# Kernel optimization log

Hardware: AMD Instinct MI355X
Metric: run time of the kernel (lower is better)

## Reference

```python
import jax, jax.numpy as jnp
import numpy as np

NEG_BIG = 1e9  # additive mask magnitude from the original code


def setup_inputs() -> dict:
    key = jax.random.key(0)
    k1, k2, k3 = jax.random.split(key, 3)
    B, H, W, Cqk, Cv = 4, 64, 64, 256, 256
    return {
        "query": jax.random.normal(k1, (B, H, W, Cqk), dtype=jnp.float32),
        "key": jax.random.normal(k2, (B, H, W, Cqk), dtype=jnp.float32),
        "value": jax.random.normal(k3, (B, H, W, Cv), dtype=jnp.float32),
    }


def reference(query, key, value):
    B = query.shape[0]
    Cqk = key.shape[-1]
    Cv = value.shape[-1]
    out_spatial = query.shape[1:-1]

    q = query.reshape(B, -1, Cqk)   # [B, Sq, C]
    k = key.reshape(B, -1, Cqk)     # [B, S, C]
    v = value.reshape(B, -1, Cv)    # [B, S, Cv]
    Sq = q.shape[1]

    # PixelSNAIL causal mask: position i may attend to strictly earlier
    # positions j < i (row 0 attends to nothing -> zero output row).
    allowed = jnp.tril(jnp.ones((Sq, Sq), dtype=q.dtype), k=-1)  # [Sq, S]

    scale = 1.0 / jnp.sqrt(jnp.asarray(Cqk, dtype=q.dtype))
    scores = jnp.einsum("bqc,bkc->bqk", q, k) * scale  # [B, Sq, S]
    scores = scores - NEG_BIG * (1.0 - allowed)
    probs = jax.nn.softmax(scores, axis=-1) * allowed   # zero out masked probs
    mixed = jnp.einsum("bqk,bkv->bqv", probs, v)        # [B, Sq, Cv]
    return mixed.reshape((B,) + out_spatial + (Cv,))
```

## Files before the change

### kernel.cpp

```cpp
#include <hip/hip_runtime.h>

#define S_LEN 4096
#define DIM   256
#define QBLK  128
#define KVBLK 64
#define TILE_SH (KVBLK * DIM)
#define PER_B  1056
#define NBLK   256

typedef __attribute__((ext_vector_type(4))) float f32x4;
typedef __attribute__((ext_vector_type(8))) short bf16x8;
typedef __attribute__((ext_vector_type(4))) unsigned short u16x4;
typedef __attribute__((ext_vector_type(8))) unsigned short u16x8;

__device__ __forceinline__ unsigned short f2bf(float x) {
    union { float f; unsigned u; } v; v.f = x;
    unsigned r = v.u + 0x7FFFu + ((v.u >> 16) & 1u);
    return (unsigned short)(r >> 16);
}
__device__ __forceinline__ float bf2f(unsigned short h) {
    union { unsigned u; float f; } v; v.u = ((unsigned)h) << 16;
    return v.f;
}

__device__ __forceinline__ void g2l16(const unsigned short* g, unsigned short* s) {
    __builtin_amdgcn_global_load_lds(
        (const __attribute__((address_space(1))) unsigned int*)g,
        (__attribute__((address_space(3))) unsigned int*)s, 16, 0, 0);
}

__device__ __forceinline__ void decode_item(int x, int& b, int& qt, int& t) {
    b = x / PER_B;
    int r = x - b * PER_B;
    int q = (int)((__fsqrt_rn(4.0f * (float)r + 1.0f) - 1.0f) * 0.5f);
    while ((q + 1) * (q + 2) <= r) ++q;
    while (q * (q + 1) > r) --q;
    qt = q;
    t = r - q * (q + 1);
}

__global__ __launch_bounds__(256) void prepass(
        const float* __restrict__ K, const float* __restrict__ V,
        unsigned short* __restrict__ KW, unsigned short* __restrict__ VW) {
    __shared__ unsigned short vt[TILE_SH];
    const int tile = blockIdx.x;
    const int tid  = threadIdx.x;
    const float* ks = K + (size_t)tile * (KVBLK * DIM);
    const float* vs = V + (size_t)tile * (KVBLK * DIM);

    char* kw = (char*)(KW + (size_t)tile * TILE_SH);
#pragma unroll
    for (int j = 0; j < 8; ++j) {
        int u = j * 256 + tid;
        int row = u >> 5, c8 = u & 31;
        f32x4 a  = *(const f32x4*)(ks + row * DIM + c8 * 8);
        f32x4 bb = *(const f32x4*)(ks + row * DIM + c8 * 8 + 4);
        u16x8 h;
        h[0] = f2bf(a[0]);  h[1] = f2bf(a[1]);  h[2] = f2bf(a[2]);  h[3] = f2bf(a[3]);
        h[4] = f2bf(bb[0]); h[5] = f2bf(bb[1]); h[6] = f2bf(bb[2]); h[7] = f2bf(bb[3]);
        unsigned off = (unsigned)(row * 512 + c8 * 16) ^ (unsigned)((row & 7) << 4);
        *(u16x8*)(kw + off) = h;
    }
    {
        int col = tid;
#pragma unroll
        for (int r8 = 0; r8 < 8; ++r8) {
            u16x8 h;
#pragma unroll
            for (int e = 0; e < 8; ++e) h[e] = f2bf(vs[(r8 * 8 + e) * DIM + col]);
            unsigned off = (unsigned)(col * 128 + r8 * 16) ^ (unsigned)((col & 7) << 4);
            *(u16x8*)((char*)vt + off) = h;
        }
    }
    __syncthreads();
    char* vw = (char*)(VW + (size_t)tile * TILE_SH);
#pragma unroll
    for (int j = 0; j < 8; ++j) {
        int u = j * 256 + tid;
        *(u16x8*)(vw + u * 16) = *(const u16x8*)((const char*)vt + u * 16);
    }
}

template<bool PACKED>
__global__ __launch_bounds__(512, 1) void attn_flash(
        const float* __restrict__ Qg, const unsigned short* __restrict__ KW,
        const unsigned short* __restrict__ VW, unsigned short* __restrict__ OP,
        float* __restrict__ ML, float* __restrict__ Og) {
    __shared__ unsigned short Ksh[2][TILE_SH];
    __shared__ unsigned short VshT[2][TILE_SH];
    __shared__ unsigned short Psh[8][16 * KVBLK];

    const int tid = threadIdx.x;
    const int w   = tid >> 6;
    const int l   = tid & 63;
    const int l15 = l & 15;
    const int lg  = l >> 4;

    int s, e;
    if (PACKED) {
        const int i = blockIdx.x;
        s = (33 * i) >> 1;
        e = (33 * (i + 1)) >> 1;
    } else {
        const int b0 = blockIdx.x & 3, q0 = blockIdx.x >> 2;
        s = b0 * PER_B + q0 * (q0 + 1);
        e = s + 2 * q0 + 2;
    }

    int b, qt, t;
    decode_item(s, b, qt, t);
    int tstart = t;
    bool firstSec = true;

    bf16x8 qf[8];
    {
        const float* qp = Qg + (size_t)(b * S_LEN + qt * QBLK + w * 16 + l15) * DIM + lg * 8;
#pragma unroll
        for (int ks = 0; ks < 8; ++ks) {
            f32x4 a = *(const f32x4*)(qp + ks * 32);
            f32x4 c = *(const f32x4*)(qp + ks * 32 + 4);
            bf16x8 f;
            f[0] = (short)f2bf(a[0] * 0.0625f); f[1] = (short)f2bf(a[1] * 0.0625f);
            f[2] = (short)f2bf(a[2] * 0.0625f); f[3] = (short)f2bf(a[3] * 0.0625f);
            f[4] = (short)f2bf(c[0] * 0.0625f); f[5] = (short)f2bf(c[1] * 0.0625f);
            f[6] = (short)f2bf(c[2] * 0.0625f); f[7] = (short)f2bf(c[3] * 0.0625f);
            qf[ks] = f;
        }
    }

    f32x4 acc[16];
#pragma unroll
    for (int i = 0; i < 16; ++i) acc[i] = (f32x4)0.0f;
    float mrun = -1e30f, lrun = 0.f;

    {
        const unsigned short* kimg = KW + (size_t)(b * 64 + t) * TILE_SH + w * 2048 + l * 8;
        const unsigned short* vimg = VW + (size_t)(b * 64 + t) * TILE_SH + w * 2048 + l * 8;
        unsigned short* kd = &Ksh[0][w * 2048];
        unsigned short* vd = &VshT[0][w * 2048];
#pragma unroll
        for (int i = 0; i < 4; ++i) {
            g2l16(kimg + i * 512, kd + i * 512);
            g2l16(vimg + i * 512, vd + i * 512);
        }
    }
    __syncthreads();

    int x = s, cur = 0;
    while (true) {
        const bool have_next = (x + 1 < e);
        int nb = b, nqt = qt, ntt = t + 1;
        const bool secEnd = !have_next || (ntt >= 2 * qt + 2);
        if (have_next) {
            if (ntt >= 2 * qt + 2) decode_item(x + 1, nb, nqt, ntt);
            const unsigned short* kimg = KW + (size_t)(nb * 64 + ntt) * TILE_SH + w * 2048 + l * 8;
            const unsigned short* vimg = VW + (size_t)(nb * 64 + ntt) * TILE_SH + w * 2048 + l * 8;
            unsigned short* kd = &Ksh[cur ^ 1][w * 2048];
            unsigned short* vd = &VshT[cur ^ 1][w * 2048];
#pragma unroll
            for (int i = 0; i < 4; ++i) {
                g2l16(kimg + i * 512, kd + i * 512);
                g2l16(vimg + i * 512, vd + i * 512);
            }
        }

        const int wqlo = qt * QBLK + w * 16;
        const bool skip = (t * KVBLK >= wqlo + 16);
        const bool msk  = (t * KVBLK + KVBLK - 1 >= wqlo);

        if (!skip) {
            f32x4 sacc[4];
#pragma unroll
            for (int j = 0; j < 4; ++j) sacc[j] = (f32x4)0.0f;
#pragma unroll
            for (int ks = 0; ks < 8; ++ks) {
#pragma unroll
                for (int jt = 0; jt < 4; ++jt) {
                    int j = jt * 16 + l15;
                    unsigned off = (unsigned)(j * 512 + (ks * 32 + lg * 8) * 2);
                    off ^= (unsigned)((j & 7) << 4);
                    bf16x8 kb = *(const bf16x8*)((const char*)Ksh[cur] + off);
                    sacc[jt] = __builtin_amdgcn_mfma_f32_16x16x32_bf16(kb, qf[ks], sacc[jt], 0, 0, 0);
                }
            }
            if (msk) {
                const int qg = wqlo + l15;
#pragma unroll
                for (int jt = 0; jt < 4; ++jt)
#pragma unroll
                    for (int rr = 0; rr < 4; ++rr) {
                        int kg = t * KVBLK + jt * 16 + lg * 4 + rr;
                        if (kg >= qg) sacc[jt][rr] = -3e38f;
                    }
            }
            {
                float m0 = fmaxf(fmaxf(sacc[0][0], sacc[0][1]), fmaxf(sacc[0][2], sacc[0][3]));
                float m1 = fmaxf(fmaxf(sacc[1][0], sacc[1][1]), fmaxf(sacc[1][2], sacc[1][3]));
                float m2 = fmaxf(fmaxf(sacc[2][0], sacc[2][1]), fmaxf(sacc[2][2], sacc[2][3]));
                float m3 = fmaxf(fmaxf(sacc[3][0], sacc[3][1]), fmaxf(sacc[3][2], sacc[3][3]));
                float mx = fmaxf(fmaxf(m0, m1), fmaxf(m2, m3));
                mx = fmaxf(mx, __shfl_xor(mx, 16));
                mx = fmaxf(mx, __shfl_xor(mx, 32));
                float mnew = fmaxf(mrun, mx);
                float corr = __expf(mrun - mnew);
                mrun = mnew;
                float ls = 0.f;
#pragma unroll
                for (int jt = 0; jt < 4; ++jt)
#pragma unroll
                    for (int rr = 0; rr < 4; ++rr) {
                        float p = __expf(sacc[jt][rr] - mnew);
                        sacc[jt][rr] = p;
                        ls += p;
                    }
                ls += __shfl_xor(ls, 16);
                ls += __shfl_xor(ls, 32);
                lrun = lrun * corr + ls;
#pragma unroll
                for (int nt = 0; nt < 16; ++nt) acc[nt] *= corr;
            }
            {
                char* pw = (char*)&Psh[w][0];
                unsigned base = (unsigned)(l15 * 128 + lg * 8) ^ (unsigned)((l15 & 7) << 4);
#pragma unroll
                for (int jt = 0; jt < 4; ++jt) {
                    u16x4 pk;
                    pk.x = f2bf(sacc[jt][0]); pk.y = f2bf(sacc[jt][1]);
                    pk.z = f2bf(sacc[jt][2]); pk.w = f2bf(sacc[jt][3]);
                    *(u16x4*)(pw + (base ^ (unsigned)(jt * 32))) = pk;
                }
            }
#pragma unroll
            for (int ks = 0; ks < 2; ++ks) {
                unsigned poff = (unsigned)(l15 * 128 + ks * 64 + lg * 16);
                poff ^= (unsigned)((l15 & 7) << 4);
                bf16x8 pb = *(const bf16x8*)((const char*)&Psh[w][0] + poff);
#pragma unroll
                for (int nt = 0; nt < 16; ++nt) {
                    unsigned voff = (unsigned)((nt * 16 + l15) * 128 + ks * 64 + lg * 16);
                    voff ^= (unsigned)((l15 & 7) << 4);
                    bf16x8 va = *(const bf16x8*)((const char*)VshT[cur] + voff);
                    acc[nt] = __builtin_amdgcn_mfma_f32_16x16x32_bf16(va, pb, acc[nt], 0, 0, 0);
                }
            }
        }
        __syncthreads();

        if (secEnd) {
            const bool complete = (tstart == 0) && (t == 2 * qt + 1);
            if (complete) {
                float rl = (lrun > 0.f) ? (1.0f / lrun) : 0.f;
                float* ob = Og + (size_t)(b * S_LEN + wqlo + l15) * DIM;
#pragma unroll
                for (int nt = 0; nt < 16; ++nt) {
                    f32x4 o = acc[nt] * rl;
                    *(f32x4*)(ob + nt * 16 + lg * 4) = o;
                }
            } else {
                const int slot = 2 * blockIdx.x + (firstSec ? 0 : 1);
                unsigned short* op = OP + (size_t)slot * (QBLK * DIM)
                                        + (size_t)(w * 16 + l15) * DIM;
#pragma unroll
                for (int nt = 0; nt < 16; ++nt) {
                    u16x4 ph;
                    ph.x = f2bf(acc[nt][0]); ph.y = f2bf(acc[nt][1]);
                    ph.z = f2bf(acc[nt][2]); ph.w = f2bf(acc[nt][3]);
                    *(u16x4*)(op + nt * 16 + lg * 4) = ph;
                }
                if (lg == 0) {
                    float* mlp = ML + (size_t)slot * (2 * QBLK);
                    mlp[(w * 16 + l15) * 2]     = mrun;
                    mlp[(w * 16 + l15) * 2 + 1] = lrun;
                }
            }
            if (!have_next) break;
            {
                const float* qp = Qg + (size_t)(nb * S_LEN + nqt * QBLK + w * 16 + l15) * DIM + lg * 8;
#pragma unroll
                for (int ks = 0; ks < 8; ++ks) {
                    f32x4 a = *(const f32x4*)(qp + ks * 32);
                    f32x4 c = *(const f32x4*)(qp + ks * 32 + 4);
                    bf16x8 f;
                    f[0] = (short)f2bf(a[0] * 0.0625f); f[1] = (short)f2bf(a[1] * 0.0625f);
                    f[2] = (short)f2bf(a[2] * 0.0625f); f[3] = (short)f2bf(a[3] * 0.0625f);
                    f[4] = (short)f2bf(c[0] * 0.0625f); f[5] = (short)f2bf(c[1] * 0.0625f);
                    f[6] = (short)f2bf(c[2] * 0.0625f); f[7] = (short)f2bf(c[3] * 0.0625f);
                    qf[ks] = f;
                }
            }
#pragma unroll
            for (int i = 0; i < 16; ++i) acc[i] = (f32x4)0.0f;
            mrun = -1e30f; lrun = 0.f;
            firstSec = false; tstart = 0;
        }
        ++x; b = nb; qt = nqt; t = ntt; cur ^= 1;
    }
}

__global__ __launch_bounds__(256) void attn_combine(
        const unsigned short* __restrict__ OP, const float* __restrict__ ML,
        float* __restrict__ Og) {
    const int id = blockIdx.x;
    const int rg = id & 3;
    const int bq = id >> 2;
    const int b  = bq >> 5;
    const int qt = bq & 31;
    const int A  = b * PER_B + qt * (qt + 1);
    const int E  = A + 2 * qt + 2;
    const int j0 = (2 * A + 1) / 33;
    const int j1 = (2 * E - 1) / 33;
    if (j0 >= j1) return;
    const int C = j1 - j0 + 1;

    int slots[6];
    for (int c = 0; c < C; ++c) {
        int j  = j0 + c;
        int sj = (33 * j) >> 1;
        slots[c] = 2 * j + ((sj >= A) ? 0 : 1);
    }

    const int tid = threadIdx.x;
    float* outb = Og + ((size_t)(b * S_LEN + qt * QBLK)) * DIM;
#pragma unroll
    for (int jj = 0; jj < 4; ++jj) {
        int u   = jj * 256 + tid;
        int row = rg * 32 + (u >> 5);
        int d8  = u & 31;
        float M = -1e30f;
        for (int c = 0; c < C; ++c)
            M = fmaxf(M, ML[(size_t)slots[c] * (2 * QBLK) + row * 2]);
        float L = 0.f;
        float o[8];
#pragma unroll
        for (int e2 = 0; e2 < 8; ++e2) o[e2] = 0.f;
        for (int c = 0; c < C; ++c) {
            float mm = ML[(size_t)slots[c] * (2 * QBLK) + row * 2];
            float ll = ML[(size_t)slots[c] * (2 * QBLK) + row * 2 + 1];
            float sc = __expf(mm - M);
            L += ll * sc;
            u16x8 ph = *(const u16x8*)(OP + ((size_t)slots[c] * QBLK + row) * DIM + d8 * 8);
#pragma unroll
            for (int e2 = 0; e2 < 8; ++e2) o[e2] += sc * bf2f(ph[e2]);
        }
        float rl = (L > 0.f) ? (1.0f / L) : 0.f;
        f32x4 o0, o1;
        o0[0] = o[0] * rl; o0[1] = o[1] * rl; o0[2] = o[2] * rl; o0[3] = o[3] * rl;
        o1[0] = o[4] * rl; o1[1] = o[5] * rl; o1[2] = o[6] * rl; o1[3] = o[7] * rl;
        *(f32x4*)(outb + (size_t)row * DIM + d8 * 8)     = o0;
        *(f32x4*)(outb + (size_t)row * DIM + d8 * 8 + 4) = o1;
    }
}

extern "C" void kernel_launch(void* const* d_in, const int* in_sizes, int n_in,
                              void* d_out, int out_size, void* d_ws, size_t ws_size,
                              hipStream_t stream) {
    const float* q = (const float*)d_in[0];
    const float* k = (const float*)d_in[1];
    const float* v = (const float*)d_in[2];
    float* o = (float*)d_out;

    const size_t imgShorts = (size_t)256 * TILE_SH;
    const size_t IMG = 2 * imgShorts * sizeof(unsigned short);
    unsigned short* KW = (unsigned short*)d_ws;
    unsigned short* VW = KW + imgShorts;

    const int nslots = 2 * NBLK;
    const size_t need = IMG
        + (size_t)nslots * (QBLK * DIM) * 2
        + (size_t)nslots * (2 * QBLK) * 4;
    if (ws_size < IMG) return;

    hipLaunchKernelGGL(prepass, dim3(256), dim3(256), 0, stream, k, v, KW, VW);
    if (ws_size >= need) {
        unsigned short* OP = (unsigned short*)((char*)d_ws + IMG);
        float* ML = (float*)(OP + (size_t)nslots * (QBLK * DIM));
        hipLaunchKernelGGL((attn_flash<true>), dim3(NBLK), dim3(512), 0, stream,
                           q, KW, VW, OP, ML, o);
        hipLaunchKernelGGL(attn_combine, dim3(512), dim3(256), 0, stream,
                           OP, ML, o);
    } else {
        hipLaunchKernelGGL((attn_flash<false>), dim3(128), dim3(512), 0, stream,
                           q, KW, VW, (unsigned short*)nullptr, (float*)nullptr, o);
    }
}
```

Before: 108.0 us.

## Double query tile per block so each K/V tile serves two query subtiles

Raises the query block from 128 to 256 rows, with each wave now holding two 16-row query fragments. Each K tile loaded into LDS is reused for twice as many MFMA score products, which roughly halves K/V global-to-LDS traffic per unit of work. The work-item decoding, stream-K style split and combine kernel are re-derived for the new tiling, and the block count is now chosen at runtime from workspace size. The cost is doubled accumulator registers per wave and coarser causal-mask granularity, so more masked work is wasted along the diagonal.

```diff
diff --git a/kernel.cpp b/kernel.cpp
--- a/kernel.cpp
+++ b/kernel.cpp
@@ -2,11 +2,11 @@
 
 #define S_LEN 4096
 #define DIM   256
-#define QBLK  128
+#define QBLK  256
 #define KVBLK 64
 #define TILE_SH (KVBLK * DIM)
-#define PER_B  1056
-#define NBLK   256
+#define PER_B  544
+#define TOT    2176
 
 typedef __attribute__((ext_vector_type(4))) float f32x4;
 typedef __attribute__((ext_vector_type(8))) short bf16x8;
@@ -32,11 +32,25 @@
 __device__ __forceinline__ void decode_item(int x, int& b, int& qt, int& t) {
     b = x / PER_B;
     int r = x - b * PER_B;
-    int q = (int)((__fsqrt_rn(4.0f * (float)r + 1.0f) - 1.0f) * 0.5f);
-    while ((q + 1) * (q + 2) <= r) ++q;
-    while (q * (q + 1) > r) --q;
+    int q = (int)((__builtin_sqrtf(2.0f * (float)r + 1.0f) - 1.0f) * 0.5f);
+    while (2 * (q + 1) * (q + 2) <= r) ++q;
+    while (2 * q * (q + 1) > r) --q;
     qt = q;
-    t = r - q * (q + 1);
+    t = r - 2 * q * (q + 1);
+}
+
+__device__ __forceinline__ void load_q(const float* qp, bf16x8* qf) {
+#pragma unroll
+    for (int ks = 0; ks < 8; ++ks) {
+        f32x4 a = *(const f32x4*)(qp + ks * 32);
+        f32x4 c = *(const f32x4*)(qp + ks * 32 + 4);
+        bf16x8 f;
+        f[0] = (short)f2bf(a[0] * 0.0625f); f[1] = (short)f2bf(a[1] * 0.0625f);
+        f[2] = (short)f2bf(a[2] * 0.0625f); f[3] = (short)f2bf(a[3] * 0.0625f);
+        f[4] = (short)f2bf(c[0] * 0.0625f); f[5] = (short)f2bf(c[1] * 0.0625f);
+        f[6] = (short)f2bf(c[2] * 0.0625f); f[7] = (short)f2bf(c[3] * 0.0625f);
+        qf[ks] = f;
+    }
 }
 
 __global__ __launch_bounds__(256) void prepass(
@@ -81,11 +95,11 @@
     }
 }
 
-template<bool PACKED>
+template<int MODE>
 __global__ __launch_bounds__(512, 1) void attn_flash(
         const float* __restrict__ Qg, const unsigned short* __restrict__ KW,
         const unsigned short* __restrict__ VW, unsigned short* __restrict__ OP,
-        float* __restrict__ ML, float* __restrict__ Og) {
+        float* __restrict__ ML, float* __restrict__ Og, int NBLK) {
     __shared__ unsigned short Ksh[2][TILE_SH];
     __shared__ unsigned short VshT[2][TILE_SH];
     __shared__ unsigned short Psh[8][16 * KVBLK];
@@ -97,14 +111,14 @@
     const int lg  = l >> 4;
 
     int s, e;
-    if (PACKED) {
+    if (MODE == 0) {
         const int i = blockIdx.x;
-        s = (33 * i) >> 1;
-        e = (33 * (i + 1)) >> 1;
+        s = (int)(((long long)TOT * i) / NBLK);
+        e = (int)(((long long)TOT * (i + 1)) / NBLK);
     } else {
         const int b0 = blockIdx.x & 3, q0 = blockIdx.x >> 2;
-        s = b0 * PER_B + q0 * (q0 + 1);
-        e = s + 2 * q0 + 2;
+        s = b0 * PER_B + 2 * q0 * (q0 + 1);
+        e = s + 4 * q0 + 4;
     }
 
     int b, qt, t;
@@ -112,26 +126,19 @@
     int tstart = t;
     bool firstSec = true;
 
-    bf16x8 qf[8];
-    {
-        const float* qp = Qg + (size_t)(b * S_LEN + qt * QBLK + w * 16 + l15) * DIM + lg * 8;
-#pragma unroll
-        for (int ks = 0; ks < 8; ++ks) {
-            f32x4 a = *(const f32x4*)(qp + ks * 32);
-            f32x4 c = *(const f32x4*)(qp + ks * 32 + 4);
-            bf16x8 f;
-            f[0] = (short)f2bf(a[0] * 0.0625f); f[1] = (short)f2bf(a[1] * 0.0625f);
-            f[2] = (short)f2bf(a[2] * 0.0625f); f[3] = (short)f2bf(a[3] * 0.0625f);
-            f[4] = (short)f2bf(c[0] * 0.0625f); f[5] = (short)f2bf(c[1] * 0.0625f);
-            f[6] = (short)f2bf(c[2] * 0.0625f); f[7] = (short)f2bf(c[3] * 0.0625f);
-            qf[ks] = f;
-        }
-    }
-
-    f32x4 acc[16];
-#pragma unroll
-    for (int i = 0; i < 16; ++i) acc[i] = (f32x4)0.0f;
-    float mrun = -1e30f, lrun = 0.f;
+    bf16x8 qf[2][8];
+#pragma unroll
+    for (int qh = 0; qh < 2; ++qh)
+        load_q(Qg + (size_t)(b * S_LEN + qt * QBLK + w * 32 + qh * 16 + l15) * DIM + lg * 8,
+               qf[qh]);
+
+    f32x4 acc[2][16];
+#pragma unroll
+    for (int qh = 0; qh < 2; ++qh)
+#pragma unroll
+        for (int i2 = 0; i2 < 16; ++i2) acc[qh][i2] = (f32x4)0.0f;
+    float mrun[2] = {-1e30f, -1e30f};
+    float lrun[2] = {0.f, 0.f};
 
     {
         const unsigned short* kimg = KW + (size_t)(b * 64 + t) * TILE_SH + w * 2048 + l * 8;
@@ -139,9 +146,9 @@
         unsigned short* kd = &Ksh[0][w * 2048];
         unsigned short* vd = &VshT[0][w * 2048];
 #pragma unroll
-        for (int i = 0; i < 4; ++i) {
-            g2l16(kimg + i * 512, kd + i * 512);
-            g2l16(vimg + i * 512, vd + i * 512);
+        for (int i2 = 0; i2 < 4; ++i2) {
+            g2l16(kimg + i2 * 512, kd + i2 * 512);
+            g2l16(vimg + i2 * 512, vd + i2 * 512);
         }
     }
     __syncthreads();
@@ -150,28 +157,30 @@
     while (true) {
         const bool have_next = (x + 1 < e);
         int nb = b, nqt = qt, ntt = t + 1;
-        const bool secEnd = !have_next || (ntt >= 2 * qt + 2);
+        const bool secEnd = !have_next || (ntt >= 4 * qt + 4);
         if (have_next) {
-            if (ntt >= 2 * qt + 2) decode_item(x + 1, nb, nqt, ntt);
+            if (ntt >= 4 * qt + 4) decode_item(x + 1, nb, nqt, ntt);
             const unsigned short* kimg = KW + (size_t)(nb * 64 + ntt) * TILE_SH + w * 2048 + l * 8;
             const unsigned short* vimg = VW + (size_t)(nb * 64 + ntt) * TILE_SH + w * 2048 + l * 8;
             unsigned short* kd = &Ksh[cur ^ 1][w * 2048];
             unsigned short* vd = &VshT[cur ^ 1][w * 2048];
 #pragma unroll
-            for (int i = 0; i < 4; ++i) {
-                g2l16(kimg + i * 512, kd + i * 512);
-                g2l16(vimg + i * 512, vd + i * 512);
+            for (int i2 = 0; i2 < 4; ++i2) {
+                g2l16(kimg + i2 * 512, kd + i2 * 512);
+                g2l16(vimg + i2 * 512, vd + i2 * 512);
             }
         }
 
-        const int wqlo = qt * QBLK + w * 16;
-        const bool skip = (t * KVBLK >= wqlo + 16);
+        const int wqlo = qt * QBLK + w * 32;
+        const bool skip = (t * KVBLK >= wqlo + 31);
         const bool msk  = (t * KVBLK + KVBLK - 1 >= wqlo);
 
         if (!skip) {
-            f32x4 sacc[4];
-#pragma unroll
-            for (int j = 0; j < 4; ++j) sacc[j] = (f32x4)0.0f;
+            f32x4 sacc[2][4];
+#pragma unroll
+            for (int qh = 0; qh < 2; ++qh)
+#pragma unroll
+                for (int j = 0; j < 4; ++j) sacc[qh][j] = (f32x4)0.0f;
 #pragma unroll
             for (int ks = 0; ks < 8; ++ks) {
 #pragma unroll
@@ -180,117 +189,128 @@
                     unsigned off = (unsigned)(j * 512 + (ks * 32 + lg * 8) * 2);
                     off ^= (unsigned)((j & 7) << 4);
                     bf16x8 kb = *(const bf16x8*)((const char*)Ksh[cur] + off);
-                    sacc[jt] = __builtin_amdgcn_mfma_f32_16x16x32_bf16(kb, qf[ks], sacc[jt], 0, 0, 0);
+                    sacc[0][jt] = __builtin_amdgcn_mfma_f32_16x16x32_bf16(kb, qf[0][ks], sacc[0][jt], 0, 0, 0);
+                    sacc[1][jt] = __builtin_amdgcn_mfma_f32_16x16x32_bf16(kb, qf[1][ks], sacc[1][jt], 0, 0, 0);
                 }
             }
-            if (msk) {
-                const int qg = wqlo + l15;
-#pragma unroll
-                for (int jt = 0; jt < 4; ++jt)
-#pragma unroll
-                    for (int rr = 0; rr < 4; ++rr) {
-                        int kg = t * KVBLK + jt * 16 + lg * 4 + rr;
-                        if (kg >= qg) sacc[jt][rr] = -3e38f;
-                    }
-            }
-            {
-                float m0 = fmaxf(fmaxf(sacc[0][0], sacc[0][1]), fmaxf(sacc[0][2], sacc[0][3]));
-                float m1 = fmaxf(fmaxf(sacc[1][0], sacc[1][1]), fmaxf(sacc[1][2], sacc[1][3]));
-                float m2 = fmaxf(fmaxf(sacc[2][0], sacc[2][1]), fmaxf(sacc[2][2], sacc[2][3]));
-                float m3 = fmaxf(fmaxf(sacc[3][0], sacc[3][1]), fmaxf(sacc[3][2], sacc[3][3]));
-                float mx = fmaxf(fmaxf(m0, m1), fmaxf(m2, m3));
-                mx = fmaxf(mx, __shfl_xor(mx, 16));
-                mx = fmaxf(mx, __shfl_xor(mx, 32));
-                float mnew = fmaxf(mrun, mx);
-                float corr = __expf(mrun - mnew);
-                mrun = mnew;
-                float ls = 0.f;
-#pragma unroll
-                for (int jt = 0; jt < 4; ++jt)
-#pragma unroll
-                    for (int rr = 0; rr < 4; ++rr) {
-                        float p = __expf(sacc[jt][rr] - mnew);
-                        sacc[jt][rr] = p;
-                        ls += p;
-                    }
-                ls += __shfl_xor(ls, 16);
-                ls += __shfl_xor(ls, 32);
-                lrun = lrun * corr + ls;
-#pragma unroll
-                for (int nt = 0; nt < 16; ++nt) acc[nt] *= corr;
-            }
-            {
-                char* pw = (char*)&Psh[w][0];
-                unsigned base = (unsigned)(l15 * 128 + lg * 8) ^ (unsigned)((l15 & 7) << 4);
-#pragma unroll
-                for (int jt = 0; jt < 4; ++jt) {
-                    u16x4 pk;
-                    pk.x = f2bf(sacc[jt][0]); pk.y = f2bf(sacc[jt][1]);
-                    pk.z = f2bf(sacc[jt][2]); pk.w = f2bf(sacc[jt][3]);
-                    *(u16x4*)(pw + (base ^ (unsigned)(jt * 32))) = pk;
+
+#pragma unroll
+            for (int qh = 0; qh < 2; ++qh) {
+                const bool act = (t * KVBLK < wqlo + qh * 16 + 15);
+                if (act) {
+                    if (msk) {
+                        const int qg = wqlo + qh * 16 + l15;
+#pragma unroll
+                        for (int jt = 0; jt < 4; ++jt)
+#pragma unroll
+                            for (int rr = 0; rr < 4; ++rr) {
+                                int kg = t * KVBLK + jt * 16 + lg * 4 + rr;
+                                if (kg >= qg) sacc[qh][jt][rr] = -3e38f;
+                            }
+                    }
+                    {
+                        float m0 = fmaxf(fmaxf(sacc[qh][0][0], sacc[qh][0][1]), fmaxf(sacc[qh][0][2], sacc[qh][0][3]));
+                        float m1 = fmaxf(fmaxf(sacc[qh][1][0], sacc[qh][1][1]), fmaxf(sacc[qh][1][2], sacc[qh][1][3]));
+                        float m2 = fmaxf(fmaxf(sacc[qh][2][0], sacc[qh][2][1]), fmaxf(sacc[qh][2][2], sacc[qh][2][3]));
+                        float m3 = fmaxf(fmaxf(sacc[qh][3][0], sacc[qh][3][1]), fmaxf(sacc[qh][3][2], sacc[qh][3][3]));
+                        float mx = fmaxf(fmaxf(m0, m1), fmaxf(m2, m3));
+                        mx = fmaxf(mx, __shfl_xor(mx, 16));
+                        mx = fmaxf(mx, __shfl_xor(mx, 32));
+                        float mnew = fmaxf(mrun[qh], mx);
+                        float corr = __expf(mrun[qh] - mnew);
+                        mrun[qh] = mnew;
+                        float ls = 0.f;
+#pragma unroll
+                        for (int jt = 0; jt < 4; ++jt)
+#pragma unroll
+                            for (int rr = 0; rr < 4; ++rr) {
+                                float p = __expf(sacc[qh][jt][rr] - mnew);
+                                sacc[qh][jt][rr] = p;
+                                ls += p;
+                            }
+                        ls += __shfl_xor(ls, 16);
+                        ls += __shfl_xor(ls, 32);
+                        lrun[qh] = lrun[qh] * corr + ls;
+#pragma unroll
+                        for (int nt = 0; nt < 16; ++nt) acc[qh][nt] *= corr;
+                    }
+                    {
+                        char* pw = (char*)&Psh[w][0];
+                        unsigned base = (unsigned)(l15 * 128 + lg * 8) ^ (unsigned)((l15 & 7) << 4);
+#pragma unroll
+                        for (int jt = 0; jt < 4; ++jt) {
+                            u16x4 pk;
+                            pk.x = f2bf(sacc[qh][jt][0]); pk.y = f2bf(sacc[qh][jt][1]);
+                            pk.z = f2bf(sacc[qh][jt][2]); pk.w = f2bf(sacc[qh][jt][3]);
+                            *(u16x4*)(pw + (base ^ (unsigned)(jt * 32))) = pk;
+                        }
+                    }
+#pragma unroll
+                    for (int ks = 0; ks < 2; ++ks) {
+                        unsigned poff = (unsigned)(l15 * 128 + ks * 64 + lg * 16);
+                        poff ^= (unsigned)((l15 & 7) << 4);
+                        bf16x8 pb = *(const bf16x8*)((const char*)&Psh[w][0] + poff);
+#pragma unroll
+                        for (int nt = 0; nt < 16; ++nt) {
+                            unsigned voff = (unsigned)((nt * 16 + l15) * 128 + ks * 64 + lg * 16);
+                            voff ^= (unsigned)((l15 & 7) << 4);
+                            bf16x8 va = *(const bf16x8*)((const char*)VshT[cur] + voff);
+                            acc[qh][nt] = __builtin_amdgcn_mfma_f32_16x16x32_bf16(va, pb, acc[qh][nt], 0, 0, 0);
+                        }
+                    }
                 }
             }
-#pragma unroll
-            for (int ks = 0; ks < 2; ++ks) {
-                unsigned poff = (unsigned)(l15 * 128 + ks * 64 + lg * 16);
-                poff ^= (unsigned)((l15 & 7) << 4);
-                bf16x8 pb = *(const bf16x8*)((const char*)&Psh[w][0] + poff);
-#pragma unroll
-                for (int nt = 0; nt < 16; ++nt) {
-                    unsigned voff = (unsigned)((nt * 16 + l15) * 128 + ks * 64 + lg * 16);
-                    voff ^= (unsigned)((l15 & 7) << 4);
-                    bf16x8 va = *(const bf16x8*)((const char*)VshT[cur] + voff);
-                    acc[nt] = __builtin_amdgcn_mfma_f32_16x16x32_bf16(va, pb, acc[nt], 0, 0, 0);
-                }
-            }
         }
         __syncthreads();
 
         if (secEnd) {
-            const bool complete = (tstart == 0) && (t == 2 * qt + 1);
+            const bool complete = (tstart == 0) && (t == 4 * qt + 3);
             if (complete) {
-                float rl = (lrun > 0.f) ? (1.0f / lrun) : 0.f;
-                float* ob = Og + (size_t)(b * S_LEN + wqlo + l15) * DIM;
-#pragma unroll
-                for (int nt = 0; nt < 16; ++nt) {
-                    f32x4 o = acc[nt] * rl;
-                    *(f32x4*)(ob + nt * 16 + lg * 4) = o;
+#pragma unroll
+                for (int qh = 0; qh < 2; ++qh) {
+                    float rl = (lrun[qh] > 0.f) ? (1.0f / lrun[qh]) : 0.f;
+                    float* ob = Og + (size_t)(b * S_LEN + wqlo + qh * 16 + l15) * DIM;
+#pragma unroll
+                    for (int nt = 0; nt < 16; ++nt) {
+                        f32x4 o = acc[qh][nt] * rl;
+                        *(f32x4*)(ob + nt * 16 + lg * 4) = o;
+                    }
                 }
             } else {
                 const int slot = 2 * blockIdx.x + (firstSec ? 0 : 1);
-                unsigned short* op = OP + (size_t)slot * (QBLK * DIM)
-                                        + (size_t)(w * 16 + l15) * DIM;
-#pragma unroll
-                for (int nt = 0; nt < 16; ++nt) {
-                    u16x4 ph;
-                    ph.x = f2bf(acc[nt][0]); ph.y = f2bf(acc[nt][1]);
-                    ph.z = f2bf(acc[nt][2]); ph.w = f2bf(acc[nt][3]);
-                    *(u16x4*)(op + nt * 16 + lg * 4) = ph;
+#pragma unroll
+                for (int qh = 0; qh < 2; ++qh) {
+                    unsigned short* op = OP + (size_t)slot * (QBLK * DIM)
+                                            + (size_t)(w * 32 + qh * 16 + l15) * DIM;
+#pragma unroll
+                    for (int nt = 0; nt < 16; ++nt) {
+                        u16x4 ph;
+                        ph.x = f2bf(acc[qh][nt][0]); ph.y = f2bf(acc[qh][nt][1]);
+                        ph.z = f2bf(acc[qh][nt][2]); ph.w = f2bf(acc[qh][nt][3]);
+                        *(u16x4*)(op + nt * 16 + lg * 4) = ph;
+                    }
                 }
                 if (lg == 0) {
                     float* mlp = ML + (size_t)slot * (2 * QBLK);
-                    mlp[(w * 16 + l15) * 2]     = mrun;
-                    mlp[(w * 16 + l15) * 2 + 1] = lrun;
+#pragma unroll
+                    for (int qh = 0; qh < 2; ++qh) {
+                        int row = w * 32 + qh * 16 + l15;
+                        mlp[row * 2]     = mrun[qh];
+                        mlp[row * 2 + 1] = lrun[qh];
+                    }
                 }
             }
             if (!have_next) break;
-            {
-                const float* qp = Qg + (size_t)(nb * S_LEN + nqt * QBLK + w * 16 + l15) * DIM + lg * 8;
-#pragma unroll
-                for (int ks = 0; ks < 8; ++ks) {
-                    f32x4 a = *(const f32x4*)(qp + ks * 32);
-                    f32x4 c = *(const f32x4*)(qp + ks * 32 + 4);
-                    bf16x8 f;
-                    f[0] = (short)f2bf(a[0] * 0.0625f); f[1] = (short)f2bf(a[1] * 0.0625f);
-                    f[2] = (short)f2bf(a[2] * 0.0625f); f[3] = (short)f2bf(a[3] * 0.0625f);
-                    f[4] = (short)f2bf(c[0] * 0.0625f); f[5] = (short)f2bf(c[1] * 0.0625f);
-                    f[6] = (short)f2bf(c[2] * 0.0625f); f[7] = (short)f2bf(c[3] * 0.0625f);
-                    qf[ks] = f;
-                }
-            }
-#pragma unroll
-            for (int i = 0; i < 16; ++i) acc[i] = (f32x4)0.0f;
-            mrun = -1e30f; lrun = 0.f;
+#pragma unroll
+            for (int qh = 0; qh < 2; ++qh)
+                load_q(Qg + (size_t)(nb * S_LEN + nqt * QBLK + w * 32 + qh * 16 + l15) * DIM + lg * 8,
+                       qf[qh]);
+#pragma unroll
+            for (int qh = 0; qh < 2; ++qh)
+#pragma unroll
+                for (int i2 = 0; i2 < 16; ++i2) acc[qh][i2] = (f32x4)0.0f;
+            mrun[0] = mrun[1] = -1e30f;
+            lrun[0] = lrun[1] = 0.f;
             firstSec = false; tstart = 0;
         }
         ++x; b = nb; qt = nqt; t = ntt; cur ^= 1;
@@ -299,25 +319,18 @@
 
 __global__ __launch_bounds__(256) void attn_combine(
         const unsigned short* __restrict__ OP, const float* __restrict__ ML,
-        float* __restrict__ Og) {
+        float* __restrict__ Og, int NBLK) {
     const int id = blockIdx.x;
-    const int rg = id & 3;
-    const int bq = id >> 2;
-    const int b  = bq >> 5;
-    const int qt = bq & 31;
-    const int A  = b * PER_B + qt * (qt + 1);
-    const int E  = A + 2 * qt + 2;
-    const int j0 = (2 * A + 1) / 33;
-    const int j1 = (2 * E - 1) / 33;
+    const int rg = id & 7;
+    const int bq = id >> 3;
+    const int b  = bq >> 4;
+    const int qt = bq & 15;
+    const int A  = b * PER_B + 2 * qt * (qt + 1);
+    const int E  = A + 4 * qt + 4;
+    const int j0 = (int)(((long long)NBLK * (A + 1) - 1) / TOT);
+    const int j1 = (int)(((long long)NBLK * E - 1) / TOT);
     if (j0 >= j1) return;
     const int C = j1 - j0 + 1;
-
-    int slots[6];
-    for (int c = 0; c < C; ++c) {
-        int j  = j0 + c;
-        int sj = (33 * j) >> 1;
-        slots[c] = 2 * j + ((sj >= A) ? 0 : 1);
-    }
 
     const int tid = threadIdx.x;
     float* outb = Og + ((size_t)(b * S_LEN + qt * QBLK)) * DIM;
@@ -327,18 +340,25 @@
         int row = rg * 32 + (u >> 5);
         int d8  = u & 31;
         float M = -1e30f;
-        for (int c = 0; c < C; ++c)
-            M = fmaxf(M, ML[(size_t)slots[c] * (2 * QBLK) + row * 2]);
+        for (int c = 0; c < C; ++c) {
+            int j  = j0 + c;
+            int sj = (int)(((long long)TOT * j) / NBLK);
+            int slot = 2 * j + ((sj >= A) ? 0 : 1);
+            M = fmaxf(M, ML[(size_t)slot * (2 * QBLK) + row * 2]);
+        }
         float L = 0.f;
         float o[8];
 #pragma unroll
         for (int e2 = 0; e2 < 8; ++e2) o[e2] = 0.f;
         for (int c = 0; c < C; ++c) {
-            float mm = ML[(size_t)slots[c] * (2 * QBLK) + row * 2];
-            float ll = ML[(size_t)slots[c] * (2 * QBLK) + row * 2 + 1];
+            int j  = j0 + c;
+            int sj = (int)(((long long)TOT * j) / NBLK);
+            int slot = 2 * j + ((sj >= A) ? 0 : 1);
+            float mm = ML[(size_t)slot * (2 * QBLK) + row * 2];
+            float ll = ML[(size_t)slot * (2 * QBLK) + row * 2 + 1];
             float sc = __expf(mm - M);
             L += ll * sc;
-            u16x8 ph = *(const u16x8*)(OP + ((size_t)slots[c] * QBLK + row) * DIM + d8 * 8);
+            u16x8 ph = *(const u16x8*)(OP + ((size_t)slot * QBLK + row) * DIM + d8 * 8);
 #pragma unroll
             for (int e2 = 0; e2 < 8; ++e2) o[e2] += sc * bf2f(ph[e2]);
         }
@@ -364,22 +384,24 @@
     unsigned short* KW = (unsigned short*)d_ws;
     unsigned short* VW = KW + imgShorts;
 
-    const int nslots = 2 * NBLK;
-    const size_t need = IMG
-        + (size_t)nslots * (QBLK * DIM) * 2
-        + (size_t)nslots * (2 * QBLK) * 4;
+    int NBLK = 0;
+    for (int nb : {256, 176}) {
+        const size_t nslots = 2 * (size_t)nb;
+        const size_t need = IMG + nslots * (QBLK * DIM) * 2 + nslots * (2 * QBLK) * 4;
+        if (ws_size >= need) { NBLK = nb; break; }
+    }
     if (ws_size < IMG) return;
 
     hipLaunchKernelGGL(prepass, dim3(256), dim3(256), 0, stream, k, v, KW, VW);
-    if (ws_size >= need) {
+    if (NBLK) {
         unsigned short* OP = (unsigned short*)((char*)d_ws + IMG);
-        float* ML = (float*)(OP + (size_t)nslots * (QBLK * DIM));
-        hipLaunchKernelGGL((attn_flash<true>), dim3(NBLK), dim3(512), 0, stream,
-                           q, KW, VW, OP, ML, o);
+        float* ML = (float*)(OP + (size_t)(2 * NBLK) * (QBLK * DIM));
+        hipLaunchKernelGGL((attn_flash<0>), dim3(NBLK), dim3(512), 0, stream,
+                           q, KW, VW, OP, ML, o, NBLK);
         hipLaunchKernelGGL(attn_combine, dim3(512), dim3(256), 0, stream,
-                           OP, ML, o);
+                           OP, ML, o, NBLK);
     } else {
-        hipLaunchKernelGGL((attn_flash<false>), dim3(128), dim3(512), 0, stream,
-                           q, KW, VW, (unsigned short*)nullptr, (float*)nullptr, o);
-    }
-}
+        hipLaunchKernelGGL((attn_flash<1>), dim3(64), dim3(512), 0, stream,
+                           q, KW, VW, (unsigned short*)nullptr, (float*)nullptr, o, 0);
+    }
+}
```

Measured after the change: 279.9 us. +159.2%, slower.

## Single-buffer K/V tiles for two blocks per CU and split work over more blocks

Applied to the files above, without the earlier changes.

Removes the LDS double buffer for K and V so each block uses roughly half the shared memory, and raises launch bounds to allow two 512-thread blocks per CU. The packed work split becomes a general TOT/NBLK partition with 512 blocks (falling back to 436 if the workspace is small), and the combine kernel recomputes slot indices inline. The intent is to hide load latency through cross-block occupancy instead of intra-block prefetch. In exchange it adds a sync and an unoverlapped load per tile, more partial-result slots to combine, and a tighter register budget that may cause spills.

```diff
diff --git a/kernel.cpp b/kernel.cpp
--- a/kernel.cpp
+++ b/kernel.cpp
@@ -6,7 +6,7 @@
 #define KVBLK 64
 #define TILE_SH (KVBLK * DIM)
 #define PER_B  1056
-#define NBLK   256
+#define TOT    4224
 
 typedef __attribute__((ext_vector_type(4))) float f32x4;
 typedef __attribute__((ext_vector_type(8))) short bf16x8;
@@ -32,7 +32,7 @@
 __device__ __forceinline__ void decode_item(int x, int& b, int& qt, int& t) {
     b = x / PER_B;
     int r = x - b * PER_B;
-    int q = (int)((__fsqrt_rn(4.0f * (float)r + 1.0f) - 1.0f) * 0.5f);
+    int q = (int)((__builtin_sqrtf(4.0f * (float)r + 1.0f) - 1.0f) * 0.5f);
     while ((q + 1) * (q + 2) <= r) ++q;
     while (q * (q + 1) > r) --q;
     qt = q;
@@ -81,13 +81,13 @@
     }
 }
 
-template<bool PACKED>
-__global__ __launch_bounds__(512, 1) void attn_flash(
+template<int MODE>
+__global__ __launch_bounds__(512, 2) void attn_flash(
         const float* __restrict__ Qg, const unsigned short* __restrict__ KW,
         const unsigned short* __restrict__ VW, unsigned short* __restrict__ OP,
-        float* __restrict__ ML, float* __restrict__ Og) {
-    __shared__ unsigned short Ksh[2][TILE_SH];
-    __shared__ unsigned short VshT[2][TILE_SH];
+        float* __restrict__ ML, float* __restrict__ Og, int NBLK) {
+    __shared__ unsigned short Ksh[TILE_SH];
+    __shared__ unsigned short VshT[TILE_SH];
     __shared__ unsigned short Psh[8][16 * KVBLK];
 
     const int tid = threadIdx.x;
@@ -97,10 +97,10 @@
     const int lg  = l >> 4;
 
     int s, e;
-    if (PACKED) {
+    if (MODE == 0) {
         const int i = blockIdx.x;
-        s = (33 * i) >> 1;
-        e = (33 * (i + 1)) >> 1;
+        s = (int)(((long long)TOT * i) / NBLK);
+        e = (int)(((long long)TOT * (i + 1)) / NBLK);
     } else {
         const int b0 = blockIdx.x & 3, q0 = blockIdx.x >> 2;
         s = b0 * PER_B + q0 * (q0 + 1);
@@ -133,36 +133,25 @@
     for (int i = 0; i < 16; ++i) acc[i] = (f32x4)0.0f;
     float mrun = -1e30f, lrun = 0.f;
 
-    {
-        const unsigned short* kimg = KW + (size_t)(b * 64 + t) * TILE_SH + w * 2048 + l * 8;
-        const unsigned short* vimg = VW + (size_t)(b * 64 + t) * TILE_SH + w * 2048 + l * 8;
-        unsigned short* kd = &Ksh[0][w * 2048];
-        unsigned short* vd = &VshT[0][w * 2048];
-#pragma unroll
-        for (int i = 0; i < 4; ++i) {
-            g2l16(kimg + i * 512, kd + i * 512);
-            g2l16(vimg + i * 512, vd + i * 512);
-        }
-    }
-    __syncthreads();
-
-    int x = s, cur = 0;
+    int x = s;
     while (true) {
+        {
+            const unsigned short* kimg = KW + (size_t)(b * 64 + t) * TILE_SH + w * 2048 + l * 8;
+            const unsigned short* vimg = VW + (size_t)(b * 64 + t) * TILE_SH + w * 2048 + l * 8;
+            unsigned short* kd = &Ksh[w * 2048];
+            unsigned short* vd = &VshT[w * 2048];
+#pragma unroll
+            for (int i2 = 0; i2 < 4; ++i2) {
+                g2l16(kimg + i2 * 512, kd + i2 * 512);
+                g2l16(vimg + i2 * 512, vd + i2 * 512);
+            }
+        }
+        __syncthreads();
+
         const bool have_next = (x + 1 < e);
         int nb = b, nqt = qt, ntt = t + 1;
         const bool secEnd = !have_next || (ntt >= 2 * qt + 2);
-        if (have_next) {
-            if (ntt >= 2 * qt + 2) decode_item(x + 1, nb, nqt, ntt);
-            const unsigned short* kimg = KW + (size_t)(nb * 64 + ntt) * TILE_SH + w * 2048 + l * 8;
-            const unsigned short* vimg = VW + (size_t)(nb * 64 + ntt) * TILE_SH + w * 2048 + l * 8;
-            unsigned short* kd = &Ksh[cur ^ 1][w * 2048];
-            unsigned short* vd = &VshT[cur ^ 1][w * 2048];
-#pragma unroll
-            for (int i = 0; i < 4; ++i) {
-                g2l16(kimg + i * 512, kd + i * 512);
-                g2l16(vimg + i * 512, vd + i * 512);
-            }
-        }
+        if (have_next && ntt >= 2 * qt + 2) decode_item(x + 1, nb, nqt, ntt);
 
         const int wqlo = qt * QBLK + w * 16;
         const bool skip = (t * KVBLK >= wqlo + 16);
@@ -179,7 +168,7 @@
                     int j = jt * 16 + l15;
                     unsigned off = (unsigned)(j * 512 + (ks * 32 + lg * 8) * 2);
                     off ^= (unsigned)((j & 7) << 4);
-                    bf16x8 kb = *(const bf16x8*)((const char*)Ksh[cur] + off);
+                    bf16x8 kb = *(const bf16x8*)((const char*)Ksh + off);
                     sacc[jt] = __builtin_amdgcn_mfma_f32_16x16x32_bf16(kb, qf[ks], sacc[jt], 0, 0, 0);
                 }
             }
@@ -239,7 +228,7 @@
                 for (int nt = 0; nt < 16; ++nt) {
                     unsigned voff = (unsigned)((nt * 16 + l15) * 128 + ks * 64 + lg * 16);
                     voff ^= (unsigned)((l15 & 7) << 4);
-                    bf16x8 va = *(const bf16x8*)((const char*)VshT[cur] + voff);
+                    bf16x8 va = *(const bf16x8*)((const char*)VshT + voff);
                     acc[nt] = __builtin_amdgcn_mfma_f32_16x16x32_bf16(va, pb, acc[nt], 0, 0, 0);
                 }
             }
@@ -289,17 +278,17 @@
                 }
             }
 #pragma unroll
-            for (int i = 0; i < 16; ++i) acc[i] = (f32x4)0.0f;
+            for (int i2 = 0; i2 < 16; ++i2) acc[i2] = (f32x4)0.0f;
             mrun = -1e30f; lrun = 0.f;
             firstSec = false; tstart = 0;
         }
-        ++x; b = nb; qt = nqt; t = ntt; cur ^= 1;
+        ++x; b = nb; qt = nqt; t = ntt;
     }
 }
 
 __global__ __launch_bounds__(256) void attn_combine(
         const unsigned short* __restrict__ OP, const float* __restrict__ ML,
-        float* __restrict__ Og) {
+        float* __restrict__ Og, int NBLK) {
     const int id = blockIdx.x;
     const int rg = id & 3;
     const int bq = id >> 2;
@@ -307,17 +296,10 @@
     const int qt = bq & 31;
     const int A  = b * PER_B + qt * (qt + 1);
     const int E  = A + 2 * qt + 2;
-    const int j0 = (2 * A + 1) / 33;
-    const int j1 = (2 * E - 1) / 33;
+    const int j0 = (int)(((long long)NBLK * (A + 1) - 1) / TOT);
+    const int j1 = (int)(((long long)NBLK * E - 1) / TOT);
     if (j0 >= j1) return;
     const int C = j1 - j0 + 1;
-
-    int slots[6];
-    for (int c = 0; c < C; ++c) {
-        int j  = j0 + c;
-        int sj = (33 * j) >> 1;
-        slots[c] = 2 * j + ((sj >= A) ? 0 : 1);
-    }
 
     const int tid = threadIdx.x;
     float* outb = Og + ((size_t)(b * S_LEN + qt * QBLK)) * DIM;
@@ -327,18 +309,25 @@
         int row = rg * 32 + (u >> 5);
         int d8  = u & 31;
         float M = -1e30f;
-        for (int c = 0; c < C; ++c)
-            M = fmaxf(M, ML[(size_t)slots[c] * (2 * QBLK) + row * 2]);
+        for (int c = 0; c < C; ++c) {
+            int j  = j0 + c;
+            int sj = (int)(((long long)TOT * j) / NBLK);
+            int slot = 2 * j + ((sj >= A) ? 0 : 1);
+            M = fmaxf(M, ML[(size_t)slot * (2 * QBLK) + row * 2]);
+        }
         float L = 0.f;
         float o[8];
 #pragma unroll
         for (int e2 = 0; e2 < 8; ++e2) o[e2] = 0.f;
         for (int c = 0; c < C; ++c) {
-            float mm = ML[(size_t)slots[c] * (2 * QBLK) + row * 2];
-            float ll = ML[(size_t)slots[c] * (2 * QBLK) + row * 2 + 1];
+            int j  = j0 + c;
+            int sj = (int)(((long long)TOT * j) / NBLK);
+            int slot = 2 * j + ((sj >= A) ? 0 : 1);
+            float mm = ML[(size_t)slot * (2 * QBLK) + row * 2];
+            float ll = ML[(size_t)slot * (2 * QBLK) + row * 2 + 1];
             float sc = __expf(mm - M);
             L += ll * sc;
-            u16x8 ph = *(const u16x8*)(OP + ((size_t)slots[c] * QBLK + row) * DIM + d8 * 8);
+            u16x8 ph = *(const u16x8*)(OP + ((size_t)slot * QBLK + row) * DIM + d8 * 8);
 #pragma unroll
             for (int e2 = 0; e2 < 8; ++e2) o[e2] += sc * bf2f(ph[e2]);
         }
@@ -364,22 +353,24 @@
     unsigned short* KW = (unsigned short*)d_ws;
     unsigned short* VW = KW + imgShorts;
 
-    const int nslots = 2 * NBLK;
-    const size_t need = IMG
-        + (size_t)nslots * (QBLK * DIM) * 2
-        + (size_t)nslots * (2 * QBLK) * 4;
+    int NBLK = 0;
+    for (int nb : {512, 436}) {
+        const size_t nslots = 2 * (size_t)nb;
+        const size_t need = IMG + nslots * ((size_t)QBLK * DIM * 2 + 2 * QBLK * 4);
+        if (ws_size >= need) { NBLK = nb; break; }
+    }
     if (ws_size < IMG) return;
 
     hipLaunchKernelGGL(prepass, dim3(256), dim3(256), 0, stream, k, v, KW, VW);
-    if (ws_size >= need) {
+    if (NBLK) {
         unsigned short* OP = (unsigned short*)((char*)d_ws + IMG);
-        float* ML = (float*)(OP + (size_t)nslots * (QBLK * DIM));
-        hipLaunchKernelGGL((attn_flash<true>), dim3(NBLK), dim3(512), 0, stream,
-                           q, KW, VW, OP, ML, o);
+        float* ML = (float*)(OP + (size_t)(2 * NBLK) * (QBLK * DIM));
+        hipLaunchKernelGGL((attn_flash<0>), dim3(NBLK), dim3(512), 0, stream,
+                           q, KW, VW, OP, ML, o, NBLK);
         hipLaunchKernelGGL(attn_combine, dim3(512), dim3(256), 0, stream,
-                           OP, ML, o);
+                           OP, ML, o, NBLK);
     } else {
-        hipLaunchKernelGGL((attn_flash<false>), dim3(128), dim3(512), 0, stream,
-                           q, KW, VW, (unsigned short*)nullptr, (float*)nullptr, o);
-    }
-}
+        hipLaunchKernelGGL((attn_flash<1>), dim3(128), dim3(512), 0, stream,
+                           q, KW, VW, (unsigned short*)nullptr, (float*)nullptr, o, 0);
+    }
+}
```

After: 127.3 us. 17.9% more time.

## Redistribute P fragments via ds_permute instead of LDS round-trip; add MFMA priority hints

Applied to the files above, without the earlier changes.

Replaces the per-wave shared-memory staging of the bf16 probability tile (write then read back as the MFMA B operand) with register-level lane exchange using ds_permute. This removes the Psh LDS buffer and its store/load traffic. It also wraps both MFMA loops in s_setprio raises so waves doing matrix work get scheduling priority. The risk is that the lane-mapping logic mismatches the MFMA operand layout, and that ds_permute still goes through the LDS crossbar, so the saving may be smaller than hoped.

```diff
diff --git a/kernel.cpp b/kernel.cpp
--- a/kernel.cpp
+++ b/kernel.cpp
@@ -7,6 +7,7 @@
 #define TILE_SH (KVBLK * DIM)
 #define PER_B  1056
 #define NBLK   256
+#define TOT    4224
 
 typedef __attribute__((ext_vector_type(4))) float f32x4;
 typedef __attribute__((ext_vector_type(8))) short bf16x8;
@@ -88,13 +89,17 @@
         float* __restrict__ ML, float* __restrict__ Og) {
     __shared__ unsigned short Ksh[2][TILE_SH];
     __shared__ unsigned short VshT[2][TILE_SH];
-    __shared__ unsigned short Psh[8][16 * KVBLK];
 
     const int tid = threadIdx.x;
     const int w   = tid >> 6;
     const int l   = tid & 63;
     const int l15 = l & 15;
     const int lg  = l >> 4;
+    const bool hi4 = (l & 16) != 0;
+    const bool hi5 = (l & 32) != 0;
+    const int sig0 = lg & 1, sig1 = lg >> 1;
+    const int addr0 = ((2 * sig0 + sig1) * 16 + l15) * 4;
+    const int addr1 = ((2 * (1 - sig0) + sig1) * 16 + l15) * 4;
 
     int s, e;
     if (PACKED) {
@@ -172,6 +177,7 @@
             f32x4 sacc[4];
 #pragma unroll
             for (int j = 0; j < 4; ++j) sacc[j] = (f32x4)0.0f;
+            __builtin_amdgcn_s_setprio(1);
 #pragma unroll
             for (int ks = 0; ks < 8; ++ks) {
 #pragma unroll
@@ -183,6 +189,7 @@
                     sacc[jt] = __builtin_amdgcn_mfma_f32_16x16x32_bf16(kb, qf[ks], sacc[jt], 0, 0, 0);
                 }
             }
+            __builtin_amdgcn_s_setprio(0);
             if (msk) {
                 const int qg = wqlo + l15;
 #pragma unroll
@@ -219,30 +226,45 @@
 #pragma unroll
                 for (int nt = 0; nt < 16; ++nt) acc[nt] *= corr;
             }
+            unsigned pbw[2][4];
             {
-                char* pw = (char*)&Psh[w][0];
-                unsigned base = (unsigned)(l15 * 128 + lg * 8) ^ (unsigned)((l15 & 7) << 4);
+                unsigned cA[4], cB[4];
 #pragma unroll
                 for (int jt = 0; jt < 4; ++jt) {
-                    u16x4 pk;
-                    pk.x = f2bf(sacc[jt][0]); pk.y = f2bf(sacc[jt][1]);
-                    pk.z = f2bf(sacc[jt][2]); pk.w = f2bf(sacc[jt][3]);
-                    *(u16x4*)(pw + (base ^ (unsigned)(jt * 32))) = pk;
-                }
-            }
+                    cA[jt] = ((unsigned)f2bf(sacc[jt][1]) << 16) | f2bf(sacc[jt][0]);
+                    cB[jt] = ((unsigned)f2bf(sacc[jt][3]) << 16) | f2bf(sacc[jt][2]);
+                }
+#pragma unroll
+                for (int q = 0; q < 2; ++q) {
+                    unsigned sA0 = hi4 ? cA[2 * q + 1] : cA[2 * q];
+                    unsigned zA0 = (unsigned)__builtin_amdgcn_ds_permute(addr0, (int)sA0);
+                    unsigned sA1 = hi4 ? cA[2 * q] : cA[2 * q + 1];
+                    unsigned zA1 = (unsigned)__builtin_amdgcn_ds_permute(addr1, (int)sA1);
+                    pbw[q][0] = hi5 ? zA1 : zA0;
+                    pbw[q][2] = hi5 ? zA0 : zA1;
+                    unsigned sB0 = hi4 ? cB[2 * q + 1] : cB[2 * q];
+                    unsigned zB0 = (unsigned)__builtin_amdgcn_ds_permute(addr0, (int)sB0);
+                    unsigned sB1 = hi4 ? cB[2 * q] : cB[2 * q + 1];
+                    unsigned zB1 = (unsigned)__builtin_amdgcn_ds_permute(addr1, (int)sB1);
+                    pbw[q][1] = hi5 ? zB1 : zB0;
+                    pbw[q][3] = hi5 ? zB0 : zB1;
+                }
+            }
+            __builtin_amdgcn_s_setprio(1);
 #pragma unroll
             for (int ks = 0; ks < 2; ++ks) {
-                unsigned poff = (unsigned)(l15 * 128 + ks * 64 + lg * 16);
-                poff ^= (unsigned)((l15 & 7) << 4);
-                bf16x8 pb = *(const bf16x8*)((const char*)&Psh[w][0] + poff);
+                union { unsigned u[4]; bf16x8 v; } pbu;
+                pbu.u[0] = pbw[ks][0]; pbu.u[1] = pbw[ks][1];
+                pbu.u[2] = pbw[ks][2]; pbu.u[3] = pbw[ks][3];
 #pragma unroll
                 for (int nt = 0; nt < 16; ++nt) {
                     unsigned voff = (unsigned)((nt * 16 + l15) * 128 + ks * 64 + lg * 16);
                     voff ^= (unsigned)((l15 & 7) << 4);
                     bf16x8 va = *(const bf16x8*)((const char*)VshT[cur] + voff);
-                    acc[nt] = __builtin_amdgcn_mfma_f32_16x16x32_bf16(va, pb, acc[nt], 0, 0, 0);
-                }
-            }
+                    acc[nt] = __builtin_amdgcn_mfma_f32_16x16x32_bf16(va, pbu.v, acc[nt], 0, 0, 0);
+                }
+            }
+            __builtin_amdgcn_s_setprio(0);
         }
         __syncthreads();
 
```

After: 107.5 us. About the same (-0.4%).
